# Performance work log

Hardware: AMD Instinct MI355X
Metric: run time of the kernel (lower is better)

## Reference

```python
import jax, jax.numpy as jnp
import numpy as np

H = 64   # hidden_layers
D = 1    # frame_dimension
N = 2048 # n_samples (batch)
T = 512  # seq_len


def setup_inputs() -> dict:
    key = jax.random.key(0)
    ks = jax.random.split(key, 12)
    s = 1.0 / np.sqrt(H)
    u = lambda k, shape: jax.random.uniform(k, shape, jnp.float32, -s, s)
    return {
        "y": jax.random.normal(ks[0], (N, T), dtype=jnp.float32),
        "W_ih1": u(ks[1], (4 * H, D)),
        "W_hh1": u(ks[2], (4 * H, H)),
        "b_ih1": u(ks[3], (4 * H,)),
        "b_hh1": u(ks[4], (4 * H,)),
        "W_ih2": u(ks[5], (4 * H, H)),
        "W_hh2": u(ks[6], (4 * H, H)),
        "b_ih2": u(ks[7], (4 * H,)),
        "b_hh2": u(ks[8], (4 * H,)),
        "W_lin": u(ks[9], (D, H)),
        "b_lin": u(ks[10], (D,)),
        "pre_output_len": 1,
    }


def _lstm_cell(x, h, c, W_ih, W_hh, b_ih, b_hh):
    # gates in PyTorch LSTMCell order: input, forget, cell(g), output
    g = x @ W_ih.T + b_ih + h @ W_hh.T + b_hh  # [n, 4H]
    i, f, gg, o = jnp.split(g, 4, axis=-1)
    i = jax.nn.sigmoid(i)
    f = jax.nn.sigmoid(f)
    gg = jnp.tanh(gg)
    o = jax.nn.sigmoid(o)
    c2 = f * c + i * gg
    h2 = o * jnp.tanh(c2)
    return h2, c2


def reference(y, W_ih1, W_hh1, b_ih1, b_hh1, W_ih2, W_hh2, b_ih2, b_hh2,
              W_lin, b_lin, pre_output_len):
    n = y.shape[0]
    zeros = jnp.zeros((n, H), dtype=jnp.float32)
    init = (zeros, zeros, zeros, zeros)

    def step(carry, x_t):
        h1, c1, h2, c2 = carry
        h1, c1 = _lstm_cell(x_t, h1, c1, W_ih1, W_hh1, b_ih1, b_hh1)
        h2, c2 = _lstm_cell(h1, h2, c2, W_ih2, W_hh2, b_ih2, b_hh2)
        out = h2 @ W_lin.T + b_lin  # [n, D]
        return (h1, c1, h2, c2), out

    ys = jnp.swapaxes(y, 0, 1)[:, :, None]  # [T, n, 1]
    _, outs = jax.lax.scan(step, init, ys)  # [T, n, D]
    outs = outs[pre_output_len:]            # drop first pre_output_len steps (static)
    # torch.cat along dim=1 of [n, D] chunks -> [n, (T - pre)*D]
    return jnp.transpose(outs, (1, 0, 2)).reshape(n, -1)
```

## Files before the change

kernel.cpp:

```cpp
#include <hip/hip_runtime.h>


typedef __attribute__((ext_vector_type(8))) short short8;
typedef __attribute__((ext_vector_type(4))) float f32x4;

#define XPITCH 2060
#define XP 0
#define HP 32960
#define OPR 51392
#define LDS_BYTES 84160
#define PLANE(layer, buf, hl) (HP + ((((layer) * 2 + (buf)) * 2) + (hl)) * 2304)

__device__ __forceinline__ float fast_rcp(float x) { return __builtin_amdgcn_rcpf(x); }
__device__ __forceinline__ float sigm(float x) { return fast_rcp(1.0f + __expf(-x)); }
__device__ __forceinline__ float tanh2(float x) {
  const float e = __expf(-2.0f * x);
  return fmaf(2.0f, fast_rcp(1.0f + e), -1.0f);
}
__device__ __forceinline__ unsigned short bf_rne(float f) {
  unsigned u = __float_as_uint(f);
  return (unsigned short)((u + 0x7FFFu + ((u >> 16) & 1u)) >> 16);
}
__device__ __forceinline__ void split8(const float* p, short8& hi, short8& lo) {
#pragma unroll
  for (int e = 0; e < 8; ++e) {
    float v = p[e];
    unsigned short h = bf_rne(v);
    float hf = __uint_as_float(((unsigned)h) << 16);
    hi[e] = (short)h;
    lo[e] = (short)bf_rne(v - hf);
  }
}
__device__ __forceinline__ unsigned cvt_pk(float a, float b) {
  unsigned r;
  asm("v_cvt_pk_bf16_f32 %0, %1, %2" : "=v"(r) : "v"(a), "v"(b));
  return r;
}
__device__ __forceinline__ f32x4 mfma16(short8 a, short8 b, f32x4 c) {
  return __builtin_amdgcn_mfma_f32_16x16x32_bf16(a, b, c, 0, 0, 0);
}

__global__ __launch_bounds__(512, 2) void lstm2_pipe(
    const float* __restrict__ y, const float* __restrict__ Wih1,
    const float* __restrict__ Whh1, const float* __restrict__ bih1,
    const float* __restrict__ bhh1, const float* __restrict__ Wih2,
    const float* __restrict__ Whh2, const float* __restrict__ bih2,
    const float* __restrict__ bhh2, const float* __restrict__ Wlin,
    const float* __restrict__ blin, float* __restrict__ out) {
  extern __shared__ char smem[];
  const int tid = threadIdx.x;
  const int w = tid >> 6;
  const int lane = tid & 63;
  const int g = lane >> 4;
  const int s = lane & 15;
  const int s0 = blockIdx.x * 16;

  for (int i = tid; i < 16 * 512; i += 512) {
    const int ss = i >> 9, t = i & 511;
    *(float*)(smem + XP + ss * XPITCH + t * 4) = y[(size_t)(s0 + ss) * 512 + t];
  }
  for (int i = tid; i < 18432 / 4; i += 512) *(float*)(smem + HP + i * 4) = 0.f;

  const float bl0 = blin[0];
  __syncthreads();

  if (w < 4) {
    short8 a1h[4][2], a1l[4][2];
    {
      const int row = 16 * w + s;
#pragma unroll
      for (int p = 0; p < 4; ++p)
#pragma unroll
        for (int c = 0; c < 2; ++c)
          split8(Whh1 + (size_t)(p * 64 + row) * 64 + 32 * c + 8 * g, a1h[p][c], a1l[p][c]);
    }
    float bias1c[4][4], wih1c[4][4];
#pragma unroll
    for (int p = 0; p < 4; ++p)
#pragma unroll
      for (int r = 0; r < 4; ++r) {
        const int row = p * 64 + 16 * w + 4 * g + r;
        bias1c[p][r] = bih1[row] + bhh1[row];
        wih1c[p][r] = Wih1[row];
      }
    float c1[4] = {0.f, 0.f, 0.f, 0.f};
    const int boffc0 = s * 144 + 16 * g;
    const int hoff = s * 144 + 32 * w + 8 * g;

#pragma unroll 1
    for (int k = 0; k <= 512; ++k) {
      if (k < 512) {
        const int rbuf = (k - 1) & 1;
        const int wbuf = k & 1;
        const float x = *(const float*)(smem + XP + s * XPITCH + k * 4);
        f32x4 acc[4];
#pragma unroll
        for (int p = 0; p < 4; ++p)
#pragma unroll
          for (int r = 0; r < 4; ++r) acc[p][r] = fmaf(wih1c[p][r], x, bias1c[p][r]);
#pragma unroll
        for (int c = 0; c < 2; ++c) {
          const int boff = boffc0 + 64 * c;
          const short8 Bh = *(const short8*)(smem + PLANE(0, rbuf, 0) + boff);
          const short8 Bl = *(const short8*)(smem + PLANE(0, rbuf, 1) + boff);
#pragma unroll
          for (int p = 0; p < 4; ++p) acc[p] = mfma16(a1h[p][c], Bh, acc[p]);
#pragma unroll
          for (int p = 0; p < 4; ++p) acc[p] = mfma16(a1h[p][c], Bl, acc[p]);
#pragma unroll
          for (int p = 0; p < 4; ++p) acc[p] = mfma16(a1l[p][c], Bh, acc[p]);
        }
        float h1n[4];
#pragma unroll
        for (int r = 0; r < 4; ++r) {
          const float ig = sigm(acc[0][r]), fg = sigm(acc[1][r]);
          const float gg = tanh2(acc[2][r]), og = sigm(acc[3][r]);
          c1[r] = fmaf(fg, c1[r], ig * gg);
          h1n[r] = og * tanh2(c1[r]);
        }
        const unsigned hA = cvt_pk(h1n[0], h1n[1]), hB = cvt_pk(h1n[2], h1n[3]);
        const unsigned lA = cvt_pk(h1n[0] - __uint_as_float(hA << 16),
                                   h1n[1] - __uint_as_float(hA & 0xFFFF0000u));
        const unsigned lB = cvt_pk(h1n[2] - __uint_as_float(hB << 16),
                                   h1n[3] - __uint_as_float(hB & 0xFFFF0000u));
        *(uint2*)(smem + PLANE(0, wbuf, 0) + hoff) = make_uint2(hA, hB);
        *(uint2*)(smem + PLANE(0, wbuf, 1) + hoff) = make_uint2(lA, lB);
      }
      __syncthreads();
    }
  } else {
    const int ow = w - 4;
    short8 a2h[4][4], a2l[4][4];
    {
      const int row = 16 * ow + s;
#pragma unroll
      for (int p = 0; p < 4; ++p)
#pragma unroll
        for (int c = 0; c < 4; ++c) {
          const float* src = (c < 2) ? (Wih2 + (size_t)(p * 64 + row) * 64 + 32 * c + 8 * g)
                                     : (Whh2 + (size_t)(p * 64 + row) * 64 + 32 * (c - 2) + 8 * g);
          split8(src, a2h[p][c], a2l[p][c]);
        }
    }
    float bias2c[4][4], wlinc[4];
#pragma unroll
    for (int p = 0; p < 4; ++p)
#pragma unroll
      for (int r = 0; r < 4; ++r) {
        const int row = p * 64 + 16 * ow + 4 * g + r;
        bias2c[p][r] = bih2[row] + bhh2[row];
      }
#pragma unroll
    for (int r = 0; r < 4; ++r) wlinc[r] = Wlin[16 * ow + 4 * g + r];
    float c2[4] = {0.f, 0.f, 0.f, 0.f};
    const int boffc0 = s * 144 + 16 * g;
    const int hoff = s * 144 + 32 * ow + 8 * g;

#pragma unroll 1
    for (int k = 0; k <= 512; ++k) {
      if (k >= 66 && ((k - 2) & 63) == 0) {
        const int base = k - 66;
        const int thr = ow * 64 + lane;
        const int ss = thr & 15, grp = thr >> 4;
#pragma unroll
        for (int q = 0; q < 4; ++q) {
          const int idx = base + grp * 4 + q;
          const int slot = idx & 127;
          const char* op = smem + OPR + slot * 256 + ss * 4;
          const float v = *(const float*)(op) + *(const float*)(op + 64) +
                          *(const float*)(op + 128) + *(const float*)(op + 192) + bl0;
          out[(size_t)(s0 + ss) * 511 + idx] = v;
        }
      }
      if (k >= 1) {
        const int t2 = k - 1;
        const int h1buf = (k - 1) & 1;
        const int h2rbuf = k & 1;
        const int h2wbuf = (k - 1) & 1;
        f32x4 acc[4];
#pragma unroll
        for (int p = 0; p < 4; ++p)
#pragma unroll
          for (int r = 0; r < 4; ++r) acc[p][r] = bias2c[p][r];
#pragma unroll
        for (int c = 0; c < 4; ++c) {
          const int lay = (c < 2) ? 0 : 1;
          const int buf = (c < 2) ? h1buf : h2rbuf;
          const int boff = boffc0 + 64 * (c & 1);
          const short8 Bh = *(const short8*)(smem + PLANE(lay, buf, 0) + boff);
          const short8 Bl = *(const short8*)(smem + PLANE(lay, buf, 1) + boff);
#pragma unroll
          for (int p = 0; p < 4; ++p) acc[p] = mfma16(a2h[p][c], Bh, acc[p]);
#pragma unroll
          for (int p = 0; p < 4; ++p) acc[p] = mfma16(a2h[p][c], Bl, acc[p]);
#pragma unroll
          for (int p = 0; p < 4; ++p) acc[p] = mfma16(a2l[p][c], Bh, acc[p]);
        }
        float h2n[4];
#pragma unroll
        for (int r = 0; r < 4; ++r) {
          const float ig = sigm(acc[0][r]), fg = sigm(acc[1][r]);
          const float gg = tanh2(acc[2][r]), og = sigm(acc[3][r]);
          c2[r] = fmaf(fg, c2[r], ig * gg);
          h2n[r] = og * tanh2(c2[r]);
        }
        const unsigned hA = cvt_pk(h2n[0], h2n[1]), hB = cvt_pk(h2n[2], h2n[3]);
        const unsigned lA = cvt_pk(h2n[0] - __uint_as_float(hA << 16),
                                   h2n[1] - __uint_as_float(hA & 0xFFFF0000u));
        const unsigned lB = cvt_pk(h2n[2] - __uint_as_float(hB << 16),
                                   h2n[3] - __uint_as_float(hB & 0xFFFF0000u));
        *(uint2*)(smem + PLANE(1, h2wbuf, 0) + hoff) = make_uint2(hA, hB);
        *(uint2*)(smem + PLANE(1, h2wbuf, 1) + hoff) = make_uint2(lA, lB);

        if (t2 >= 1) {
          float pw = wlinc[0] * h2n[0];
          pw = fmaf(wlinc[1], h2n[1], pw);
          pw = fmaf(wlinc[2], h2n[2], pw);
          pw = fmaf(wlinc[3], h2n[3], pw);
          pw += __shfl_xor(pw, 16, 64);
          pw += __shfl_xor(pw, 32, 64);
          if (g == 0)
            *(float*)(smem + OPR + ((t2 - 1) & 127) * 256 + ow * 64 + s * 4) = pw;
        }
      }
      __syncthreads();
    }
    {
      const int thr = ow * 64 + lane;
      for (int e = thr; e < 63 * 16; e += 256) {
        const int ss = e & 15, off = e >> 4;
        const int idx = 448 + off;
        const int slot = idx & 127;
        const char* op = smem + OPR + slot * 256 + ss * 4;
        const float v = *(const float*)(op) + *(const float*)(op + 64) +
                        *(const float*)(op + 128) + *(const float*)(op + 192) + bl0;
        out[(size_t)(s0 + ss) * 511 + idx] = v;
      }
    }
  }
}

extern "C" void kernel_launch(void* const* d_in, const int* in_sizes, int n_in,
                              void* d_out, int out_size, void* d_ws, size_t ws_size,
                              hipStream_t stream) {
  const float* y    = (const float*)d_in[0];
  const float* Wih1 = (const float*)d_in[1];
  const float* Whh1 = (const float*)d_in[2];
  const float* bih1 = (const float*)d_in[3];
  const float* bhh1 = (const float*)d_in[4];
  const float* Wih2 = (const float*)d_in[5];
  const float* Whh2 = (const float*)d_in[6];
  const float* bih2 = (const float*)d_in[7];
  const float* bhh2 = (const float*)d_in[8];
  const float* Wlin = (const float*)d_in[9];
  const float* blin = (const float*)d_in[10];
  float* out = (float*)d_out;

  hipFuncSetAttribute((const void*)lstm2_pipe,
                      hipFuncAttributeMaxDynamicSharedMemorySize, LDS_BYTES);
  lstm2_pipe<<<dim3(128), dim3(512), LDS_BYTES, stream>>>(
      y, Wih1, Whh1, bih1, bhh1, Wih2, Whh2, bih2, bhh2, Wlin, blin, out);
}
```

Before: 648.0 us.

## Fold log2 scaling into weights, fuse gate math, unroll timestep loop by two

```diff
diff --git a/kernel.cpp b/kernel.cpp
--- a/kernel.cpp
+++ b/kernel.cpp
@@ -4,27 +4,28 @@
 typedef __attribute__((ext_vector_type(8))) short short8;
 typedef __attribute__((ext_vector_type(4))) float f32x4;
 
+#define NT 512
 #define XPITCH 2060
 #define XP 0
 #define HP 32960
-#define OPR 51392
+#define RING 51392
 #define LDS_BYTES 84160
 #define PLANE(layer, buf, hl) (HP + ((((layer) * 2 + (buf)) * 2) + (hl)) * 2304)
+#define L2E 1.44269504f
+#define N2L2E (-2.8853900817779268f)
 
 __device__ __forceinline__ float fast_rcp(float x) { return __builtin_amdgcn_rcpf(x); }
-__device__ __forceinline__ float sigm(float x) { return fast_rcp(1.0f + __expf(-x)); }
-__device__ __forceinline__ float tanh2(float x) {
-  const float e = __expf(-2.0f * x);
-  return fmaf(2.0f, fast_rcp(1.0f + e), -1.0f);
+__device__ __forceinline__ float exp2_f(float x) {
+  float r; asm("v_exp_f32 %0, %1" : "=v"(r) : "v"(x)); return r;
 }
 __device__ __forceinline__ unsigned short bf_rne(float f) {
   unsigned u = __float_as_uint(f);
   return (unsigned short)((u + 0x7FFFu + ((u >> 16) & 1u)) >> 16);
 }
-__device__ __forceinline__ void split8(const float* p, short8& hi, short8& lo) {
+__device__ __forceinline__ void split8sc(const float* p, float sc, short8& hi, short8& lo) {
 #pragma unroll
   for (int e = 0; e < 8; ++e) {
-    float v = p[e];
+    float v = p[e] * sc;
     unsigned short h = bf_rne(v);
     float hf = __uint_as_float(((unsigned)h) << 16);
     hi[e] = (short)h;
@@ -39,8 +40,17 @@
 __device__ __forceinline__ f32x4 mfma16(short8 a, short8 b, f32x4 c) {
   return __builtin_amdgcn_mfma_f32_16x16x32_bf16(a, b, c, 0, 0, 0);
 }
-
-__global__ __launch_bounds__(512, 2) void lstm2_pipe(
+__device__ __forceinline__ void cell2(float i, float f, float g, float o,
+                                      float& c, float& h) {
+  const float ei = exp2_f(-i), ef = exp2_f(-f), eg = exp2_f(-g), eo = exp2_f(-o);
+  const float P = (1.f - eg) * fast_rcp((1.f + ei) * (1.f + eg));
+  c = fmaf(c, fast_rcp(1.f + ef), P);
+  const float cc = fminf(15.f, fmaxf(-15.f, c));
+  const float ec = exp2_f(N2L2E * cc);
+  h = (1.f - ec) * fast_rcp((1.f + eo) * (1.f + ec));
+}
+
+__global__ __launch_bounds__(512, 2) void lstm2_r13(
     const float* __restrict__ y, const float* __restrict__ Wih1,
     const float* __restrict__ Whh1, const float* __restrict__ bih1,
     const float* __restrict__ bhh1, const float* __restrict__ Wih2,
@@ -60,181 +70,232 @@
     *(float*)(smem + XP + ss * XPITCH + t * 4) = y[(size_t)(s0 + ss) * 512 + t];
   }
   for (int i = tid; i < 18432 / 4; i += 512) *(float*)(smem + HP + i * 4) = 0.f;
-
   const float bl0 = blin[0];
   __syncthreads();
 
+  const int bo0 = s * 144 + 16 * g, bo1 = bo0 + 64;
+  const float gsc[4] = {L2E, L2E, 2.0f * L2E, L2E};
+
   if (w < 4) {
     short8 a1h[4][2], a1l[4][2];
-    {
-      const int row = 16 * w + s;
-#pragma unroll
-      for (int p = 0; p < 4; ++p)
-#pragma unroll
-        for (int c = 0; c < 2; ++c)
-          split8(Whh1 + (size_t)(p * 64 + row) * 64 + 32 * c + 8 * g, a1h[p][c], a1l[p][c]);
-    }
+#pragma unroll
+    for (int p = 0; p < 4; ++p)
+#pragma unroll
+      for (int c = 0; c < 2; ++c)
+        split8sc(Whh1 + (size_t)(p * 64 + 16 * w + s) * 64 + 32 * c + 8 * g,
+                 gsc[p], a1h[p][c], a1l[p][c]);
     float bias1c[4][4], wih1c[4][4];
 #pragma unroll
     for (int p = 0; p < 4; ++p)
 #pragma unroll
       for (int r = 0; r < 4; ++r) {
         const int row = p * 64 + 16 * w + 4 * g + r;
-        bias1c[p][r] = bih1[row] + bhh1[row];
-        wih1c[p][r] = Wih1[row];
+        bias1c[p][r] = (bih1[row] + bhh1[row]) * gsc[p];
+        wih1c[p][r] = Wih1[row] * gsc[p];
       }
     float c1[4] = {0.f, 0.f, 0.f, 0.f};
-    const int boffc0 = s * 144 + 16 * g;
-    const int hoff = s * 144 + 32 * w + 8 * g;
-
+    const int hwr0 = s * 144 + 32 * w + 8 * g;
+
+    int eR[2][4], eW[2][2];
+#pragma unroll
+    for (int P = 0; P < 2; ++P) {
+      const int rb = P ^ 1;
+      eR[P][0] = PLANE(0, rb, 0) + bo0;
+      eR[P][1] = PLANE(0, rb, 1) + bo0;
+      eR[P][2] = PLANE(0, rb, 0) + bo1;
+      eR[P][3] = PLANE(0, rb, 1) + bo1;
+      eW[P][0] = PLANE(0, P, 0) + hwr0;
+      eW[P][1] = PLANE(0, P, 1) + hwr0;
+    }
+
+#define EBODY(KK, P)                                                          \
+  {                                                                           \
+    const float x = *(const float*)(smem + XP + s * XPITCH + (KK) * 4);       \
+    const short8 Bh0 = *(const short8*)(smem + eR[P][0]);                     \
+    const short8 Bl0 = *(const short8*)(smem + eR[P][1]);                     \
+    const short8 Bh1 = *(const short8*)(smem + eR[P][2]);                     \
+    const short8 Bl1 = *(const short8*)(smem + eR[P][3]);                     \
+    f32x4 acc[4];                                                             \
+    _Pragma("unroll") for (int p = 0; p < 4; ++p) {                           \
+      _Pragma("unroll") for (int r = 0; r < 4; ++r)                           \
+          acc[p][r] = fmaf(wih1c[p][r], x, bias1c[p][r]);                     \
+    }                                                                         \
+    __builtin_amdgcn_s_setprio(1);                                            \
+    _Pragma("unroll") for (int p = 0; p < 4; ++p)                             \
+        acc[p] = mfma16(a1h[p][0], Bh0, acc[p]);                              \
+    _Pragma("unroll") for (int p = 0; p < 4; ++p)                             \
+        acc[p] = mfma16(a1h[p][1], Bh1, acc[p]);                              \
+    _Pragma("unroll") for (int p = 0; p < 4; ++p)                             \
+        acc[p] = mfma16(a1h[p][0], Bl0, acc[p]);                              \
+    _Pragma("unroll") for (int p = 0; p < 4; ++p)                             \
+        acc[p] = mfma16(a1h[p][1], Bl1, acc[p]);                              \
+    _Pragma("unroll") for (int p = 0; p < 4; ++p)                             \
+        acc[p] = mfma16(a1l[p][0], Bh0, acc[p]);                              \
+    _Pragma("unroll") for (int p = 0; p < 4; ++p)                             \
+        acc[p] = mfma16(a1l[p][1], Bh1, acc[p]);                              \
+    __builtin_amdgcn_s_setprio(0);                                            \
+    float h1n[4];                                                             \
+    _Pragma("unroll") for (int r = 0; r < 4; ++r)                             \
+        cell2(acc[0][r], acc[1][r], acc[2][r], acc[3][r], c1[r], h1n[r]);     \
+    const unsigned hA = cvt_pk(h1n[0], h1n[1]), hB = cvt_pk(h1n[2], h1n[3]);  \
+    const unsigned lA = cvt_pk(h1n[0] - __uint_as_float(hA << 16),            \
+                               h1n[1] - __uint_as_float(hA & 0xFFFF0000u));   \
+    const unsigned lB = cvt_pk(h1n[2] - __uint_as_float(hB << 16),            \
+                               h1n[3] - __uint_as_float(hB & 0xFFFF0000u));   \
+    *(uint2*)(smem + eW[P][0]) = make_uint2(hA, hB);                          \
+    *(uint2*)(smem + eW[P][1]) = make_uint2(lA, lB);                          \
+  }
+
+    EBODY(0, 0);
+    __syncthreads();
 #pragma unroll 1
-    for (int k = 0; k <= 512; ++k) {
-      if (k < 512) {
-        const int rbuf = (k - 1) & 1;
-        const int wbuf = k & 1;
-        const float x = *(const float*)(smem + XP + s * XPITCH + k * 4);
-        f32x4 acc[4];
-#pragma unroll
-        for (int p = 0; p < 4; ++p)
-#pragma unroll
-          for (int r = 0; r < 4; ++r) acc[p][r] = fmaf(wih1c[p][r], x, bias1c[p][r]);
-#pragma unroll
-        for (int c = 0; c < 2; ++c) {
-          const int boff = boffc0 + 64 * c;
-          const short8 Bh = *(const short8*)(smem + PLANE(0, rbuf, 0) + boff);
-          const short8 Bl = *(const short8*)(smem + PLANE(0, rbuf, 1) + boff);
-#pragma unroll
-          for (int p = 0; p < 4; ++p) acc[p] = mfma16(a1h[p][c], Bh, acc[p]);
-#pragma unroll
-          for (int p = 0; p < 4; ++p) acc[p] = mfma16(a1h[p][c], Bl, acc[p]);
-#pragma unroll
-          for (int p = 0; p < 4; ++p) acc[p] = mfma16(a1l[p][c], Bh, acc[p]);
-        }
-        float h1n[4];
-#pragma unroll
-        for (int r = 0; r < 4; ++r) {
-          const float ig = sigm(acc[0][r]), fg = sigm(acc[1][r]);
-          const float gg = tanh2(acc[2][r]), og = sigm(acc[3][r]);
-          c1[r] = fmaf(fg, c1[r], ig * gg);
-          h1n[r] = og * tanh2(c1[r]);
-        }
-        const unsigned hA = cvt_pk(h1n[0], h1n[1]), hB = cvt_pk(h1n[2], h1n[3]);
-        const unsigned lA = cvt_pk(h1n[0] - __uint_as_float(hA << 16),
-                                   h1n[1] - __uint_as_float(hA & 0xFFFF0000u));
-        const unsigned lB = cvt_pk(h1n[2] - __uint_as_float(hB << 16),
-                                   h1n[3] - __uint_as_float(hB & 0xFFFF0000u));
-        *(uint2*)(smem + PLANE(0, wbuf, 0) + hoff) = make_uint2(hA, hB);
-        *(uint2*)(smem + PLANE(0, wbuf, 1) + hoff) = make_uint2(lA, lB);
-      }
+    for (int kb = 1; kb <= 509; kb += 2) {
+      EBODY(kb, 1);
       __syncthreads();
-    }
+      EBODY(kb + 1, 0);
+      __syncthreads();
+    }
+    EBODY(511, 1);
+    __syncthreads();
+    __syncthreads();
   } else {
     const int ow = w - 4;
     short8 a2h[4][4], a2l[4][4];
-    {
-      const int row = 16 * ow + s;
-#pragma unroll
-      for (int p = 0; p < 4; ++p)
-#pragma unroll
-        for (int c = 0; c < 4; ++c) {
-          const float* src = (c < 2) ? (Wih2 + (size_t)(p * 64 + row) * 64 + 32 * c + 8 * g)
-                                     : (Whh2 + (size_t)(p * 64 + row) * 64 + 32 * (c - 2) + 8 * g);
-          split8(src, a2h[p][c], a2l[p][c]);
-        }
-    }
-    float bias2c[4][4], wlinc[4];
+#pragma unroll
+    for (int p = 0; p < 4; ++p)
+#pragma unroll
+      for (int c = 0; c < 4; ++c) {
+        const float* src = (c < 2)
+            ? (Wih2 + (size_t)(p * 64 + 16 * ow + s) * 64 + 32 * c + 8 * g)
+            : (Whh2 + (size_t)(p * 64 + 16 * ow + s) * 64 + 32 * (c - 2) + 8 * g);
+        split8sc(src, gsc[p], a2h[p][c], a2l[p][c]);
+      }
+    f32x4 bias2v[4];
+    float wlinc[4];
 #pragma unroll
     for (int p = 0; p < 4; ++p)
 #pragma unroll
       for (int r = 0; r < 4; ++r) {
         const int row = p * 64 + 16 * ow + 4 * g + r;
-        bias2c[p][r] = bih2[row] + bhh2[row];
+        bias2v[p][r] = (bih2[row] + bhh2[row]) * gsc[p];
       }
 #pragma unroll
     for (int r = 0; r < 4; ++r) wlinc[r] = Wlin[16 * ow + 4 * g + r];
     float c2[4] = {0.f, 0.f, 0.f, 0.f};
-    const int boffc0 = s * 144 + 16 * g;
-    const int hoff = s * 144 + 32 * ow + 8 * g;
-
+    const int hwr0 = s * 144 + 32 * ow + 8 * g;
+    const int ringb = RING + ow * 64 + s * 4;
+
+    int oR[2][8], oW[2][2];
+#pragma unroll
+    for (int P = 0; P < 2; ++P) {
+      oR[P][0] = PLANE(0, P ^ 1, 0) + bo0;
+      oR[P][1] = PLANE(0, P ^ 1, 1) + bo0;
+      oR[P][2] = PLANE(0, P ^ 1, 0) + bo1;
+      oR[P][3] = PLANE(0, P ^ 1, 1) + bo1;
+      oR[P][4] = PLANE(1, P, 0) + bo0;
+      oR[P][5] = PLANE(1, P, 1) + bo0;
+      oR[P][6] = PLANE(1, P, 0) + bo1;
+      oR[P][7] = PLANE(1, P, 1) + bo1;
+      oW[P][0] = PLANE(1, P ^ 1, 0) + hwr0;
+      oW[P][1] = PLANE(1, P ^ 1, 1) + hwr0;
+    }
+
+#define OFLUSH(KK)                                                            \
+  if ((KK) >= 66 && (((KK)-2) & 63) == 0) {                                   \
+    const int base = (KK)-66;                                                 \
+    const int thr = ow * 64 + lane;                                           \
+    const int ss2 = thr & 15, grp = thr >> 4;                                 \
+    _Pragma("unroll") for (int q = 0; q < 4; ++q) {                           \
+      const int idx = base + grp * 4 + q;                                     \
+      const char* op = smem + RING + (idx & 127) * 256 + ss2 * 4;             \
+      const float v = *(const float*)(op) + *(const float*)(op + 64) +        \
+                      *(const float*)(op + 128) + *(const float*)(op + 192) + \
+                      bl0;                                                    \
+      out[(size_t)(s0 + ss2) * 511 + idx] = v;                                \
+    }                                                                         \
+  }
+
+#define OBODY(KK, P)                                                          \
+  {                                                                           \
+    const short8 Bh0 = *(const short8*)(smem + oR[P][0]);                     \
+    const short8 Bl0 = *(const short8*)(smem + oR[P][1]);                     \
+    const short8 Bh1 = *(const short8*)(smem + oR[P][2]);                     \
+    const short8 Bl1 = *(const short8*)(smem + oR[P][3]);                     \
+    const short8 Ch0 = *(const short8*)(smem + oR[P][4]);                     \
+    const short8 Cl0 = *(const short8*)(smem + oR[P][5]);                     \
+    const short8 Ch1 = *(const short8*)(smem + oR[P][6]);                     \
+    const short8 Cl1 = *(const short8*)(smem + oR[P][7]);                     \
+    f32x4 acc[4];                                                             \
+    __builtin_amdgcn_s_setprio(1);                                            \
+    _Pragma("unroll") for (int p = 0; p < 4; ++p)                             \
+        acc[p] = mfma16(a2h[p][0], Bh0, bias2v[p]);                           \
+    _Pragma("unroll") for (int p = 0; p < 4; ++p)                             \
+        acc[p] = mfma16(a2h[p][1], Bh1, acc[p]);                              \
+    _Pragma("unroll") for (int p = 0; p < 4; ++p)                             \
+        acc[p] = mfma16(a2h[p][0], Bl0, acc[p]);                              \
+    _Pragma("unroll") for (int p = 0; p < 4; ++p)                             \
+        acc[p] = mfma16(a2h[p][1], Bl1, acc[p]);                              \
+    _Pragma("unroll") for (int p = 0; p < 4; ++p)                             \
+        acc[p] = mfma16(a2l[p][0], Bh0, acc[p]);                              \
+    _Pragma("unroll") for (int p = 0; p < 4; ++p)                             \
+        acc[p] = mfma16(a2l[p][1], Bh1, acc[p]);                              \
+    _Pragma("unroll") for (int p = 0; p < 4; ++p)                             \
+        acc[p] = mfma16(a2h[p][2], Ch0, acc[p]);                              \
+    _Pragma("unroll") for (int p = 0; p < 4; ++p)                             \
+        acc[p] = mfma16(a2h[p][3], Ch1, acc[p]);                              \
+    _Pragma("unroll") for (int p = 0; p < 4; ++p)                             \
+        acc[p] = mfma16(a2h[p][2], Cl0, acc[p]);                              \
+    _Pragma("unroll") for (int p = 0; p < 4; ++p)                             \
+        acc[p] = mfma16(a2h[p][3], Cl1, acc[p]);                              \
+    _Pragma("unroll") for (int p = 0; p < 4; ++p)                             \
+        acc[p] = mfma16(a2l[p][2], Ch0, acc[p]);                              \
+    _Pragma("unroll") for (int p = 0; p < 4; ++p)                             \
+        acc[p] = mfma16(a2l[p][3], Ch1, acc[p]);                              \
+    __builtin_amdgcn_s_setprio(0);                                            \
+    float h2n[4];                                                             \
+    _Pragma("unroll") for (int r = 0; r < 4; ++r)                             \
+        cell2(acc[0][r], acc[1][r], acc[2][r], acc[3][r], c2[r], h2n[r]);     \
+    const unsigned hA = cvt_pk(h2n[0], h2n[1]), hB = cvt_pk(h2n[2], h2n[3]);  \
+    const unsigned lA = cvt_pk(h2n[0] - __uint_as_float(hA << 16),            \
+                               h2n[1] - __uint_as_float(hA & 0xFFFF0000u));   \
+    const unsigned lB = cvt_pk(h2n[2] - __uint_as_float(hB << 16),            \
+                               h2n[3] - __uint_as_float(hB & 0xFFFF0000u));   \
+    *(uint2*)(smem + oW[P][0]) = make_uint2(hA, hB);                          \
+    *(uint2*)(smem + oW[P][1]) = make_uint2(lA, lB);                          \
+    if ((KK) >= 2) {                                                          \
+      float pw = wlinc[0] * h2n[0];                                           \
+      pw = fmaf(wlinc[1], h2n[1], pw);                                        \
+      pw = fmaf(wlinc[2], h2n[2], pw);                                        \
+      pw = fmaf(wlinc[3], h2n[3], pw);                                        \
+      pw += __shfl_xor(pw, 16, 64);                                           \
+      pw += __shfl_xor(pw, 32, 64);                                           \
+      if (g == 0)                                                             \
+        *(float*)(smem + ringb + (((KK)-2) & 127) * 256) = pw;                \
+    }                                                                         \
+  }
+
+    __syncthreads();
 #pragma unroll 1
-    for (int k = 0; k <= 512; ++k) {
-      if (k >= 66 && ((k - 2) & 63) == 0) {
-        const int base = k - 66;
-        const int thr = ow * 64 + lane;
-        const int ss = thr & 15, grp = thr >> 4;
-#pragma unroll
-        for (int q = 0; q < 4; ++q) {
-          const int idx = base + grp * 4 + q;
-          const int slot = idx & 127;
-          const char* op = smem + OPR + slot * 256 + ss * 4;
-          const float v = *(const float*)(op) + *(const float*)(op + 64) +
-                          *(const float*)(op + 128) + *(const float*)(op + 192) + bl0;
-          out[(size_t)(s0 + ss) * 511 + idx] = v;
-        }
-      }
-      if (k >= 1) {
-        const int t2 = k - 1;
-        const int h1buf = (k - 1) & 1;
-        const int h2rbuf = k & 1;
-        const int h2wbuf = (k - 1) & 1;
-        f32x4 acc[4];
-#pragma unroll
-        for (int p = 0; p < 4; ++p)
-#pragma unroll
-          for (int r = 0; r < 4; ++r) acc[p][r] = bias2c[p][r];
-#pragma unroll
-        for (int c = 0; c < 4; ++c) {
-          const int lay = (c < 2) ? 0 : 1;
-          const int buf = (c < 2) ? h1buf : h2rbuf;
-          const int boff = boffc0 + 64 * (c & 1);
-          const short8 Bh = *(const short8*)(smem + PLANE(lay, buf, 0) + boff);
-          const short8 Bl = *(const short8*)(smem + PLANE(lay, buf, 1) + boff);
-#pragma unroll
-          for (int p = 0; p < 4; ++p) acc[p] = mfma16(a2h[p][c], Bh, acc[p]);
-#pragma unroll
-          for (int p = 0; p < 4; ++p) acc[p] = mfma16(a2h[p][c], Bl, acc[p]);
-#pragma unroll
-          for (int p = 0; p < 4; ++p) acc[p] = mfma16(a2l[p][c], Bh, acc[p]);
-        }
-        float h2n[4];
-#pragma unroll
-        for (int r = 0; r < 4; ++r) {
-          const float ig = sigm(acc[0][r]), fg = sigm(acc[1][r]);
-          const float gg = tanh2(acc[2][r]), og = sigm(acc[3][r]);
-          c2[r] = fmaf(fg, c2[r], ig * gg);
-          h2n[r] = og * tanh2(c2[r]);
-        }
-        const unsigned hA = cvt_pk(h2n[0], h2n[1]), hB = cvt_pk(h2n[2], h2n[3]);
-        const unsigned lA = cvt_pk(h2n[0] - __uint_as_float(hA << 16),
-                                   h2n[1] - __uint_as_float(hA & 0xFFFF0000u));
-        const unsigned lB = cvt_pk(h2n[2] - __uint_as_float(hB << 16),
-                                   h2n[3] - __uint_as_float(hB & 0xFFFF0000u));
-        *(uint2*)(smem + PLANE(1, h2wbuf, 0) + hoff) = make_uint2(hA, hB);
-        *(uint2*)(smem + PLANE(1, h2wbuf, 1) + hoff) = make_uint2(lA, lB);
-
-        if (t2 >= 1) {
-          float pw = wlinc[0] * h2n[0];
-          pw = fmaf(wlinc[1], h2n[1], pw);
-          pw = fmaf(wlinc[2], h2n[2], pw);
-          pw = fmaf(wlinc[3], h2n[3], pw);
-          pw += __shfl_xor(pw, 16, 64);
-          pw += __shfl_xor(pw, 32, 64);
-          if (g == 0)
-            *(float*)(smem + OPR + ((t2 - 1) & 127) * 256 + ow * 64 + s * 4) = pw;
-        }
-      }
+    for (int kb = 1; kb <= 509; kb += 2) {
+      OBODY(kb, 1);
       __syncthreads();
-    }
+      OFLUSH(kb + 1);
+      OBODY(kb + 1, 0);
+      __syncthreads();
+    }
+    OBODY(511, 1);
+    __syncthreads();
+    OBODY(512, 0);
+    __syncthreads();
     {
       const int thr = ow * 64 + lane;
       for (int e = thr; e < 63 * 16; e += 256) {
-        const int ss = e & 15, off = e >> 4;
+        const int ss2 = e & 15, off = e >> 4;
         const int idx = 448 + off;
-        const int slot = idx & 127;
-        const char* op = smem + OPR + slot * 256 + ss * 4;
+        const char* op = smem + RING + (idx & 127) * 256 + ss2 * 4;
         const float v = *(const float*)(op) + *(const float*)(op + 64) +
                         *(const float*)(op + 128) + *(const float*)(op + 192) + bl0;
-        out[(size_t)(s0 + ss) * 511 + idx] = v;
+        out[(size_t)(s0 + ss2) * 511 + idx] = v;
       }
     }
   }
@@ -256,8 +317,8 @@
   const float* blin = (const float*)d_in[10];
   float* out = (float*)d_out;
 
-  hipFuncSetAttribute((const void*)lstm2_pipe,
+  hipFuncSetAttribute((const void*)lstm2_r13,
                       hipFuncAttributeMaxDynamicSharedMemorySize, LDS_BYTES);
-  lstm2_pipe<<<dim3(128), dim3(512), LDS_BYTES, stream>>>(
+  lstm2_r13<<<dim3(128), dim3(512), LDS_BYTES, stream>>>(
       y, Wih1, Whh1, bih1, bhh1, Wih2, Whh2, bih2, bhh2, Wlin, blin, out);
 }
```

After: 636.3 us. About the same (-1.8%).
